# Kernel optimization log

Measured on AMD Instinct MI355X. Metric: run time of the kernel, lower is better.

Reference implementation:

```python
import jax, jax.numpy as jnp
import numpy as np

# Block sizes (DGL message-flow-graph / sampled blocks)
NS0, ND0, NE0 = 300000, 50000, 800000   # block0: 2-hop frontier -> 1-hop frontier
NS1, ND1, NE1 = 50000, 8192, 131072     # block1: 1-hop frontier -> seed nodes


def _graph_conv(x, src, dst, ew, W, b, n_src, n_dst, weight_first):
    """DGL GraphConv with norm='both' and edge_weight.

    x: [n_src, d_in] source-node features; (src, dst): edge endpoints;
    ew: [E] edge weights. Degrees are UNWEIGHTED (copy of DGL semantics),
    clamped to >= 1. Weight applied before aggregation iff d_in > d_out.
    """
    ones_e = jnp.ones_like(ew)
    out_deg = jnp.clip(jax.ops.segment_sum(ones_e, src, num_segments=n_src), 1.0, None)
    h = x * (out_deg ** -0.5)[:, None]
    if weight_first:
        h = h @ W
    # gather-weight-scatter: m_v = sum_{e: e->v} ew_e * h_{src_e}
    msg = jax.ops.segment_sum(ew[:, None] * h[src], dst, num_segments=n_dst)
    in_deg = jnp.clip(jax.ops.segment_sum(ones_e, dst, num_segments=n_dst), 1.0, None)
    msg = msg * (in_deg ** -0.5)[:, None]
    if not weight_first:
        msg = msg @ W
    return msg + b


def setup_inputs() -> dict:
    key = jax.random.key(0)
    ks = jax.random.split(key, 12)
    in_f, hid_f, out_f = 256, 128, 128
    return {
        "x": jax.random.normal(ks[0], (NS0, in_f), dtype=jnp.float32),
        "src0": jax.random.randint(ks[1], (NE0,), 0, NS0, dtype=jnp.int64 if jax.config.jax_enable_x64 else jnp.int32).astype(jnp.int32),
        "dst0": jax.random.randint(ks[2], (NE0,), 0, ND0).astype(jnp.int32),
        "ew0": jax.random.normal(ks[3], (NE0,), dtype=jnp.float32),
        "src1": jax.random.randint(ks[4], (NE1,), 0, NS1).astype(jnp.int32),
        "dst1": jax.random.randint(ks[5], (NE1,), 0, ND1).astype(jnp.int32),
        "ew1": jax.random.normal(ks[6], (NE1,), dtype=jnp.float32),
        "W1": jax.random.normal(ks[7], (in_f, hid_f), dtype=jnp.float32) * 0.05,
        "b1": jax.random.normal(ks[8], (hid_f,), dtype=jnp.float32) * 0.05,
        "W2": jax.random.normal(ks[9], (hid_f, out_f), dtype=jnp.float32) * 0.05,
        "b2": jax.random.normal(ks[10], (out_f,), dtype=jnp.float32) * 0.05,
    }


def reference(x, src0, dst0, ew0, src1, dst1, ew1, W1, b1, W2, b2):
    # layer 1: in(256) > hidden(128) -> weight applied before aggregation
    h = jax.nn.relu(_graph_conv(x, src0, dst0, ew0, W1, b1, NS0, ND0, weight_first=True))
    # layer 2: hidden(128) <= out(128) -> aggregate then weight
    out = jax.nn.relu(_graph_conv(h, src1, dst1, ew1, W2, b2, NS1, ND1, weight_first=False))
    return out  # [ND1, out_f]
```

## Files before the change

### kernel.cpp

```cpp
#include <hip/hip_runtime.h>

#define NS0 300000
#define ND0 50000
#define NE0 800000
#define NS1 50000
#define ND1 8192
#define NE1 131072
#define IN_F 256
#define HID_F 128
#define SLOTS 64
#define NTILE (NS0 / 16)
#define GEMM_GRID 2048
#define BUILD_GRID 512

typedef __attribute__((ext_vector_type(8))) _Float16 half8_t;
typedef __attribute__((ext_vector_type(4))) _Float16 half4_t;
typedef __attribute__((ext_vector_type(4))) float f32x4;

#define OFF_OUTDEG0I 0
#define OFF_OUTDEG1I 300000
#define OFF_CNT0     350000
#define OFF_CNT1     400000
#define ZERO_WORDS   408192
#define OFF_EDGE0    408192
#define OFF_EDGE1    6808192
#define OFF_H1       7856768
#define OFF_W1T      14256768
#define OFF_G        14273152

__global__ __launch_bounds__(256) void k_init(
    int4* __restrict__ p, const float* __restrict__ W1,
    _Float16* __restrict__ w1t) {
  if (blockIdx.x < 128) {
    int i = blockIdx.x * 256 + threadIdx.x;
    for (; i < ZERO_WORDS / 4; i += 128 * 256) p[i] = make_int4(0, 0, 0, 0);
  } else {
    int i = (blockIdx.x - 128) * 256 + threadIdx.x;
    for (; i < IN_F * HID_F; i += 32 * 256) {
      int k = i >> 7, n = i & 127;
      w1t[n * 256 + k] = (_Float16)W1[i];
    }
  }
}

#define LDB(p, o) (*reinterpret_cast<const half8_t*>((p) + (o)))
__global__ __launch_bounds__(256) void k_gemm_build(
    const float* __restrict__ x, const _Float16* __restrict__ w1t,
    _Float16* __restrict__ g,
    const int* __restrict__ src0, const int* __restrict__ dst0,
    const float* __restrict__ ew0, int* __restrict__ outdeg0,
    int* __restrict__ cnt0, int2* __restrict__ edge0,
    const int* __restrict__ src1, const int* __restrict__ dst1,
    const float* __restrict__ ew1, int* __restrict__ outdeg1,
    int* __restrict__ cnt1, int2* __restrict__ edge1) {
  __shared__ __align__(16) _Float16 ldsA[2][16 * 256];
  __shared__ _Float16 ldsT[4][16 * 40];

  if (blockIdx.x >= GEMM_GRID) {
    int tid = (blockIdx.x - GEMM_GRID) * 256 + threadIdx.x;
    int stride = BUILD_GRID * 256;
    for (int i = tid; i < NE0; i += stride) {
      int s = src0[i];
      int d = dst0[i];
      float w = ew0[i];
      atomicAdd(&outdeg0[s], 1);
      int slot = atomicAdd(&cnt0[d], 1);
      if (slot < SLOTS) edge0[d * SLOTS + slot] = make_int2(s, __float_as_int(w));
    }
    for (int i = tid; i < NE1; i += stride) {
      int s = src1[i];
      int d = dst1[i];
      float w = ew1[i];
      atomicAdd(&outdeg1[s], 1);
      int slot = atomicAdd(&cnt1[d], 1);
      if (slot < SLOTS) edge1[d * SLOTS + slot] = make_int2(s, __float_as_int(w));
    }
    return;
  }

  const int tid = threadIdx.x;
  const int wv = tid >> 6;
  const int lane = tid & 63;
  const int m = lane & 15;
  const int grp = lane >> 4;
  _Float16* tp = ldsT[wv];

  const _Float16* wb0 = w1t + (size_t)(32 * wv + m) * 256 + grp * 8;
  const _Float16* wb1 = wb0 + 16 * 256;
  const half8_t b00 = LDB(wb0, 0),   b01 = LDB(wb0, 32),  b02 = LDB(wb0, 64),
                b03 = LDB(wb0, 96),  b04 = LDB(wb0, 128), b05 = LDB(wb0, 160),
                b06 = LDB(wb0, 192), b07 = LDB(wb0, 224);
  const half8_t b10 = LDB(wb1, 0),   b11 = LDB(wb1, 32),  b12 = LDB(wb1, 64),
                b13 = LDB(wb1, 96),  b14 = LDB(wb1, 128), b15 = LDB(wb1, 160),
                b16 = LDB(wb1, 192), b17 = LDB(wb1, 224);

  const int skb = lane >> 3;
  const int sgrp = (lane >> 1) & 3;
  const int sjh = lane & 1;
  const int row_r = lane >> 2;
  const int q_r   = lane & 3;

  const int bid = blockIdx.x;
  float4 pv[4];

  {
    const float* tb = x + (size_t)bid * 4096;
#pragma unroll
    for (int r = 0; r < 4; ++r) {
      const int mr = wv + 4 * r;
      const float4 v = *reinterpret_cast<const float4*>(tb + tid * 4 + r * 1024);
      half4_t h;
      h[0] = (_Float16)v.x; h[1] = (_Float16)v.y;
      h[2] = (_Float16)v.z; h[3] = (_Float16)v.w;
      const int idx = skb * 64 + sgrp * 16 + mr;
      const int S = idx ^ skb ^ sgrp;
      *reinterpret_cast<half4_t*>(
          reinterpret_cast<char*>(&ldsA[0][0]) + S * 16 + sjh * 8) = h;
    }
  }
  __syncthreads();

  int cur = 0;
  for (int tile = bid; tile < NTILE; tile += GEMM_GRID) {
    const int nxt = tile + GEMM_GRID;
    if (nxt < NTILE) {
      const float* tb = x + (size_t)nxt * 4096;
#pragma unroll
      for (int r = 0; r < 4; ++r)
        pv[r] = *reinterpret_cast<const float4*>(tb + tid * 4 + r * 1024);
    }
    {
      const char* A = reinterpret_cast<const char*>(&ldsA[cur][0]);
      f32x4 acc0 = {0.f, 0.f, 0.f, 0.f};
      f32x4 acc1 = {0.f, 0.f, 0.f, 0.f};
#define STEP(KB, B0, B1)                                                       \
  {                                                                            \
    const int Sr = ((KB * 64 + lane) ^ KB ^ grp);                              \
    const half8_t af = *reinterpret_cast<const half8_t*>(A + Sr * 16);         \
    acc0 = __builtin_amdgcn_mfma_f32_16x16x32_f16(af, B0, acc0, 0, 0, 0);      \
    acc1 = __builtin_amdgcn_mfma_f32_16x16x32_f16(af, B1, acc1, 0, 0, 0);      \
  }
      STEP(0, b00, b10)
      STEP(1, b01, b11)
      STEP(2, b02, b12)
      STEP(3, b03, b13)
      STEP(4, b04, b14)
      STEP(5, b05, b15)
      STEP(6, b06, b16)
      STEP(7, b07, b17)
#undef STEP
#pragma unroll
      for (int r = 0; r < 4; ++r) {
        tp[(4 * grp + r) * 40 + m]      = (_Float16)acc0[r];
        tp[(4 * grp + r) * 40 + 16 + m] = (_Float16)acc1[r];
      }
      const half8_t ov =
          *reinterpret_cast<const half8_t*>(tp + row_r * 40 + q_r * 8);
      *reinterpret_cast<half8_t*>(
          g + (size_t)(tile * 16 + row_r) * 128 + 32 * wv + q_r * 8) = ov;
    }
    if (nxt < NTILE) {
      char* B = reinterpret_cast<char*>(&ldsA[cur ^ 1][0]);
#pragma unroll
      for (int r = 0; r < 4; ++r) {
        const int mr = wv + 4 * r;
        half4_t h;
        h[0] = (_Float16)pv[r].x; h[1] = (_Float16)pv[r].y;
        h[2] = (_Float16)pv[r].z; h[3] = (_Float16)pv[r].w;
        const int idx = skb * 64 + sgrp * 16 + mr;
        const int S = idx ^ skb ^ sgrp;
        *reinterpret_cast<half4_t*>(B + S * 16 + sjh * 8) = h;
      }
    }
    __syncthreads();
    cur ^= 1;
  }
}

__global__ __launch_bounds__(256) void k_gather1(
    const _Float16* __restrict__ g, const int* __restrict__ cnt,
    const int2* __restrict__ edge, const int* __restrict__ outdeg0,
    const int* __restrict__ outdeg1, const float* __restrict__ b1,
    float* __restrict__ h1) {
  const int w = (blockIdx.x * 256 + threadIdx.x) >> 6;
  const int lane = threadIdx.x & 63;
  const int gp = lane >> 4;
  const int sl = lane & 15;
  if (w >= ND0) return;
  const int deg = min(cnt[w], SLOTS);
  const int2* ep = edge + (size_t)w * SLOTS;
  float acc[8] = {0.f, 0.f, 0.f, 0.f, 0.f, 0.f, 0.f, 0.f};
  for (int e = 0; e < deg; e += 4) {
    const int idx = e + gp;
    int2 p = make_int2(0, 0);
    float c = 0.f;
    if (idx < deg) {
      p = ep[idx];
      c = __int_as_float(p.y) * rsqrtf(fmaxf((float)outdeg0[p.x], 1.0f));
    }
    const half8_t v =
        *reinterpret_cast<const half8_t*>(g + (size_t)p.x * 128 + sl * 8);
#pragma unroll
    for (int j = 0; j < 8; ++j) acc[j] = fmaf(c, (float)v[j], acc[j]);
  }
#pragma unroll
  for (int j = 0; j < 8; ++j) {
    acc[j] += __shfl_xor(acc[j], 16, 64);
    acc[j] += __shfl_xor(acc[j], 32, 64);
  }
  if (gp == 0) {
    const float sc = rsqrtf(fmaxf((float)deg, 1.0f));
    const float s1 = rsqrtf(fmaxf((float)outdeg1[w], 1.0f));
    const float4 bv0 = *reinterpret_cast<const float4*>(b1 + sl * 8);
    const float4 bv1 = *reinterpret_cast<const float4*>(b1 + sl * 8 + 4);
    float4 o0, o1;
    o0.x = fmaxf(fmaf(acc[0], sc, bv0.x), 0.0f) * s1;
    o0.y = fmaxf(fmaf(acc[1], sc, bv0.y), 0.0f) * s1;
    o0.z = fmaxf(fmaf(acc[2], sc, bv0.z), 0.0f) * s1;
    o0.w = fmaxf(fmaf(acc[3], sc, bv0.w), 0.0f) * s1;
    o1.x = fmaxf(fmaf(acc[4], sc, bv1.x), 0.0f) * s1;
    o1.y = fmaxf(fmaf(acc[5], sc, bv1.y), 0.0f) * s1;
    o1.z = fmaxf(fmaf(acc[6], sc, bv1.z), 0.0f) * s1;
    o1.w = fmaxf(fmaf(acc[7], sc, bv1.w), 0.0f) * s1;
    float* hr = h1 + (size_t)w * 128 + sl * 8;
    *reinterpret_cast<float4*>(hr) = o0;
    *reinterpret_cast<float4*>(hr + 4) = o1;
  }
}

#define FMA2(acc, c, v)        \
  acc.x = fmaf(c, v.x, acc.x); \
  acc.y = fmaf(c, v.y, acc.y);

__global__ __launch_bounds__(256) void k_layer2(
    const float* __restrict__ h1, const int* __restrict__ cnt,
    const int2* __restrict__ edge, const float* __restrict__ W2,
    const float* __restrict__ b2, float* __restrict__ out) {
  __shared__ float arow[8][HID_F];
  const int t = blockIdx.x;
  const int wv = threadIdx.x >> 6;
  const int lane = threadIdx.x & 63;

#pragma unroll
  for (int rr = 0; rr < 2; ++rr) {
    const int row = t * 8 + wv * 2 + rr;
    const int deg = min(cnt[row], SLOTS);
    const int2* ep = edge + (size_t)row * SLOTS;
    float2 acc = make_float2(0.f, 0.f);
    int e = 0;
    for (; e + 4 <= deg; e += 4) {
      int4 q0 = *reinterpret_cast<const int4*>(ep + e);
      int4 q1 = *reinterpret_cast<const int4*>(ep + e + 2);
      float2 v0 = *reinterpret_cast<const float2*>(h1 + (size_t)q0.x * HID_F + lane * 2);
      float2 v1 = *reinterpret_cast<const float2*>(h1 + (size_t)q0.z * HID_F + lane * 2);
      float2 v2 = *reinterpret_cast<const float2*>(h1 + (size_t)q1.x * HID_F + lane * 2);
      float2 v3 = *reinterpret_cast<const float2*>(h1 + (size_t)q1.z * HID_F + lane * 2);
      FMA2(acc, __int_as_float(q0.y), v0);
      FMA2(acc, __int_as_float(q0.w), v1);
      FMA2(acc, __int_as_float(q1.y), v2);
      FMA2(acc, __int_as_float(q1.w), v3);
    }
    for (; e < deg; ++e) {
      int2 p = ep[e];
      float2 v = *reinterpret_cast<const float2*>(h1 + (size_t)p.x * HID_F + lane * 2);
      FMA2(acc, __int_as_float(p.y), v);
    }
    const float sc = rsqrtf(fmaxf((float)deg, 1.0f));
    *reinterpret_cast<float2*>(&arow[wv * 2 + rr][lane * 2]) =
        make_float2(acc.x * sc, acc.y * sc);
  }
  __syncthreads();

  const int j = threadIdx.x & 127;
  const int rg = threadIdx.x >> 7;
  float a0 = 0.f, a1 = 0.f, a2 = 0.f, a3 = 0.f;
  const float* wj = W2 + j;
#pragma unroll 8
  for (int k = 0; k < HID_F; ++k) {
    const float wvv = wj[(size_t)k * 128];
    a0 = fmaf(arow[rg * 4 + 0][k], wvv, a0);
    a1 = fmaf(arow[rg * 4 + 1][k], wvv, a1);
    a2 = fmaf(arow[rg * 4 + 2][k], wvv, a2);
    a3 = fmaf(arow[rg * 4 + 3][k], wvv, a3);
  }
  const float bj = b2[j];
  const int row0 = t * 8 + rg * 4;
  out[(size_t)(row0 + 0) * 128 + j] = fmaxf(a0 + bj, 0.0f);
  out[(size_t)(row0 + 1) * 128 + j] = fmaxf(a1 + bj, 0.0f);
  out[(size_t)(row0 + 2) * 128 + j] = fmaxf(a2 + bj, 0.0f);
  out[(size_t)(row0 + 3) * 128 + j] = fmaxf(a3 + bj, 0.0f);
}

extern "C" void kernel_launch(void* const* d_in, const int* in_sizes, int n_in,
                              void* d_out, int out_size, void* d_ws, size_t ws_size,
                              hipStream_t stream) {
  const float* x    = (const float*)d_in[0];
  const int*   src0 = (const int*)d_in[1];
  const int*   dst0 = (const int*)d_in[2];
  const float* ew0  = (const float*)d_in[3];
  const int*   src1 = (const int*)d_in[4];
  const int*   dst1 = (const int*)d_in[5];
  const float* ew1  = (const float*)d_in[6];
  const float* W1   = (const float*)d_in[7];
  const float* b1   = (const float*)d_in[8];
  const float* W2   = (const float*)d_in[9];
  const float* b2   = (const float*)d_in[10];
  float* out = (float*)d_out;

  int*   wsi = (int*)d_ws;
  float* wsf = (float*)d_ws;
  int* outdeg0 = wsi + OFF_OUTDEG0I;
  int* outdeg1 = wsi + OFF_OUTDEG1I;
  int* cnt0    = wsi + OFF_CNT0;
  int* cnt1    = wsi + OFF_CNT1;
  int2* edge0  = (int2*)(wsi + OFF_EDGE0);
  int2* edge1  = (int2*)(wsi + OFF_EDGE1);
  float* h1    = wsf + OFF_H1;
  _Float16* w1t = (_Float16*)(wsi + OFF_W1T);
  _Float16* g   = (_Float16*)(wsi + OFF_G);

  k_init<<<160, 256, 0, stream>>>((int4*)d_ws, W1, w1t);
  k_gemm_build<<<GEMM_GRID + BUILD_GRID, 256, 0, stream>>>(
      x, w1t, g, src0, dst0, ew0, outdeg0, cnt0, edge0,
      src1, dst1, ew1, outdeg1, cnt1, edge1);
  k_gather1<<<(ND0 * 64) / 256, 256, 0, stream>>>(g, cnt0, edge0, outdeg0,
                                                  outdeg1, b1, h1);
  k_layer2<<<ND1 / 8, 256, 0, stream>>>(h1, cnt1, edge1, W2, b2, out);
}
```

Before: 235.7 us.

## Deepen GEMM prefetch to two tiles ahead and place build blocks first

The GEMM loop now keeps two register buffers of upcoming x tiles, so global loads run two iterations ahead of the MFMA compute instead of one. The loop is unrolled by two with static LDS buffer indices. The edge-build blocks are moved to the low block indices so they are dispatched first and overlap with the GEMM blocks. This costs more registers per thread, which can lower occupancy. The launch grid presumably still covers both roles, though that part is not shown.

```diff
diff --git a/kernel.cpp b/kernel.cpp
--- a/kernel.cpp
+++ b/kernel.cpp
@@ -56,8 +56,8 @@
   __shared__ __align__(16) _Float16 ldsA[2][16 * 256];
   __shared__ _Float16 ldsT[4][16 * 40];
 
-  if (blockIdx.x >= GEMM_GRID) {
-    int tid = (blockIdx.x - GEMM_GRID) * 256 + threadIdx.x;
+  if (blockIdx.x < BUILD_GRID) {
+    int tid = blockIdx.x * 256 + threadIdx.x;
     int stride = BUILD_GRID * 256;
     for (int i = tid; i < NE0; i += stride) {
       int s = src0[i];
@@ -100,8 +100,56 @@
   const int row_r = lane >> 2;
   const int q_r   = lane & 3;
 
-  const int bid = blockIdx.x;
-  float4 pv[4];
+  const int bid = blockIdx.x - BUILD_GRID;
+  float4 pv1[4], pv2[4];
+
+#define LOAD_PV(PV, T)                                                         \
+  {                                                                            \
+    const float* tb = x + (size_t)(T) * 4096;                                  \
+    _Pragma("unroll") for (int r = 0; r < 4; ++r)                              \
+        PV[r] = *reinterpret_cast<const float4*>(tb + tid * 4 + r * 1024);     \
+  }
+
+#define WRITE_LDS(BUFI, PV)                                                    \
+  {                                                                            \
+    char* Bp = reinterpret_cast<char*>(&ldsA[BUFI][0]);                        \
+    _Pragma("unroll") for (int r = 0; r < 4; ++r) {                            \
+      const int mr = wv + 4 * r;                                               \
+      half4_t h;                                                               \
+      h[0] = (_Float16)PV[r].x; h[1] = (_Float16)PV[r].y;                      \
+      h[2] = (_Float16)PV[r].z; h[3] = (_Float16)PV[r].w;                      \
+      const int idx = skb * 64 + sgrp * 16 + mr;                               \
+      const int S = idx ^ skb ^ sgrp;                                          \
+      *reinterpret_cast<half4_t*>(Bp + S * 16 + sjh * 8) = h;                  \
+    }                                                                          \
+  }
+
+#define STEP(A, KB, B0, B1)                                                    \
+  {                                                                            \
+    const int Sr = ((KB * 64 + lane) ^ KB ^ grp);                              \
+    const half8_t af = *reinterpret_cast<const half8_t*>(A + Sr * 16);         \
+    acc0 = __builtin_amdgcn_mfma_f32_16x16x32_f16(af, B0, acc0, 0, 0, 0);      \
+    acc1 = __builtin_amdgcn_mfma_f32_16x16x32_f16(af, B1, acc1, 0, 0, 0);      \
+  }
+
+#define COMPUTE_TILE(BUFI, T)                                                  \
+  {                                                                            \
+    const char* A = reinterpret_cast<const char*>(&ldsA[BUFI][0]);             \
+    f32x4 acc0 = {0.f, 0.f, 0.f, 0.f};                                         \
+    f32x4 acc1 = {0.f, 0.f, 0.f, 0.f};                                         \
+    STEP(A, 0, b00, b10) STEP(A, 1, b01, b11)                                  \
+    STEP(A, 2, b02, b12) STEP(A, 3, b03, b13)                                  \
+    STEP(A, 4, b04, b14) STEP(A, 5, b05, b15)                                  \
+    STEP(A, 6, b06, b16) STEP(A, 7, b07, b17)                                  \
+    _Pragma("unroll") for (int r = 0; r < 4; ++r) {                            \
+      tp[(4 * grp + r) * 40 + m]      = (_Float16)acc0[r];                     \
+      tp[(4 * grp + r) * 40 + 16 + m] = (_Float16)acc1[r];                     \
+    }                                                                          \
+    const half8_t ov =                                                         \
+        *reinterpret_cast<const half8_t*>(tp + row_r * 40 + q_r * 8);          \
+    *reinterpret_cast<half8_t*>(                                               \
+        g + (size_t)((T) * 16 + row_r) * 128 + 32 * wv + q_r * 8) = ov;        \
+  }
 
   {
     const float* tb = x + (size_t)bid * 4096;
@@ -118,63 +166,28 @@
           reinterpret_cast<char*>(&ldsA[0][0]) + S * 16 + sjh * 8) = h;
     }
   }
+  if (bid + GEMM_GRID < NTILE) LOAD_PV(pv1, bid + GEMM_GRID);
   __syncthreads();
 
-  int cur = 0;
-  for (int tile = bid; tile < NTILE; tile += GEMM_GRID) {
-    const int nxt = tile + GEMM_GRID;
-    if (nxt < NTILE) {
-      const float* tb = x + (size_t)nxt * 4096;
-#pragma unroll
-      for (int r = 0; r < 4; ++r)
-        pv[r] = *reinterpret_cast<const float4*>(tb + tid * 4 + r * 1024);
-    }
-    {
-      const char* A = reinterpret_cast<const char*>(&ldsA[cur][0]);
-      f32x4 acc0 = {0.f, 0.f, 0.f, 0.f};
-      f32x4 acc1 = {0.f, 0.f, 0.f, 0.f};
-#define STEP(KB, B0, B1)                                                       \
-  {                                                                            \
-    const int Sr = ((KB * 64 + lane) ^ KB ^ grp);                              \
-    const half8_t af = *reinterpret_cast<const half8_t*>(A + Sr * 16);         \
-    acc0 = __builtin_amdgcn_mfma_f32_16x16x32_f16(af, B0, acc0, 0, 0, 0);      \
-    acc1 = __builtin_amdgcn_mfma_f32_16x16x32_f16(af, B1, acc1, 0, 0, 0);      \
-  }
-      STEP(0, b00, b10)
-      STEP(1, b01, b11)
-      STEP(2, b02, b12)
-      STEP(3, b03, b13)
-      STEP(4, b04, b14)
-      STEP(5, b05, b15)
-      STEP(6, b06, b16)
-      STEP(7, b07, b17)
+  for (int t = bid; t < NTILE; t += 2 * GEMM_GRID) {
+    const int tA2 = t + 2 * GEMM_GRID;
+    if (tA2 < NTILE) LOAD_PV(pv2, tA2);
+    COMPUTE_TILE(0, t);
+    if (t + GEMM_GRID < NTILE) WRITE_LDS(1, pv1);
+    __syncthreads();
+    const int tB = t + GEMM_GRID;
+    if (tB < NTILE) {
+      const int tB3 = t + 3 * GEMM_GRID;
+      if (tB3 < NTILE) LOAD_PV(pv1, tB3);
+      COMPUTE_TILE(1, tB);
+      if (tA2 < NTILE) WRITE_LDS(0, pv2);
+      __syncthreads();
+    }
+  }
+#undef LOAD_PV
+#undef WRITE_LDS
 #undef STEP
-#pragma unroll
-      for (int r = 0; r < 4; ++r) {
-        tp[(4 * grp + r) * 40 + m]      = (_Float16)acc0[r];
-        tp[(4 * grp + r) * 40 + 16 + m] = (_Float16)acc1[r];
-      }
-      const half8_t ov =
-          *reinterpret_cast<const half8_t*>(tp + row_r * 40 + q_r * 8);
-      *reinterpret_cast<half8_t*>(
-          g + (size_t)(tile * 16 + row_r) * 128 + 32 * wv + q_r * 8) = ov;
-    }
-    if (nxt < NTILE) {
-      char* B = reinterpret_cast<char*>(&ldsA[cur ^ 1][0]);
-#pragma unroll
-      for (int r = 0; r < 4; ++r) {
-        const int mr = wv + 4 * r;
-        half4_t h;
-        h[0] = (_Float16)pv[r].x; h[1] = (_Float16)pv[r].y;
-        h[2] = (_Float16)pv[r].z; h[3] = (_Float16)pv[r].w;
-        const int idx = skb * 64 + sgrp * 16 + mr;
-        const int S = idx ^ skb ^ sgrp;
-        *reinterpret_cast<half4_t*>(B + S * 16 + sjh * 8) = h;
-      }
-    }
-    __syncthreads();
-    cur ^= 1;
-  }
+#undef COMPUTE_TILE
 }
 
 __global__ __launch_bounds__(256) void k_gather1(
```

Result: faster. 229.8 us (median of 2 runs) (-2.5%).

## Make GEMM wave-independent with per-wave 16-row tiles and fused edge build

Applied to the files above, without the earlier changes.

The layer-1 X·W1 GEMM is restructured so that each wavefront owns a whole 16-row tile and computes all 128 output columns. B fragments come from a pre-swizzled fp16 W1 layout in global memory/L2 rather than being held in registers. This removes the block-wide double buffer and __syncthreads. The edge-bucket build, which used to run in separate blocks, is now done by every block before its GEMM work. The trade-offs are more global loads of B per tile, no cross-tile prefetch, and atomic-heavy edge work serialized ahead of the GEMM inside each block.

```diff
diff --git a/kernel.cpp b/kernel.cpp
--- a/kernel.cpp
+++ b/kernel.cpp
@@ -10,8 +10,8 @@
 #define HID_F 128
 #define SLOTS 64
 #define NTILE (NS0 / 16)
-#define GEMM_GRID 2048
-#define BUILD_GRID 512
+#define GRID 2048
+#define TPLD 136
 
 typedef __attribute__((ext_vector_type(8))) _Float16 half8_t;
 typedef __attribute__((ext_vector_type(4))) _Float16 half4_t;
@@ -25,27 +25,31 @@
 #define OFF_EDGE0    408192
 #define OFF_EDGE1    6808192
 #define OFF_H1       7856768
-#define OFF_W1T      14256768
+#define OFF_W1X      14256768
 #define OFF_G        14273152
 
 __global__ __launch_bounds__(256) void k_init(
     int4* __restrict__ p, const float* __restrict__ W1,
-    _Float16* __restrict__ w1t) {
+    _Float16* __restrict__ w1x) {
   if (blockIdx.x < 128) {
     int i = blockIdx.x * 256 + threadIdx.x;
     for (; i < ZERO_WORDS / 4; i += 128 * 256) p[i] = make_int4(0, 0, 0, 0);
   } else {
-    int i = (blockIdx.x - 128) * 256 + threadIdx.x;
-    for (; i < IN_F * HID_F; i += 32 * 256) {
-      int k = i >> 7, n = i & 127;
-      w1t[n * 256 + k] = (_Float16)W1[i];
-    }
-  }
-}
-
-#define LDB(p, o) (*reinterpret_cast<const half8_t*>((p) + (o)))
-__global__ __launch_bounds__(256) void k_gemm_build(
-    const float* __restrict__ x, const _Float16* __restrict__ w1t,
+    int f = (blockIdx.x - 128) * 256 + threadIdx.x;
+    for (; f < IN_F * HID_F; f += 32 * 256) {
+      const int ct = f >> 12;
+      const int kb = (f >> 9) & 7;
+      const int grpm = (f >> 3) & 63;
+      const int j = f & 7;
+      const int n = ct * 16 + (grpm & 15);
+      const int k = kb * 32 + (grpm >> 4) * 8 + j;
+      w1x[f] = (_Float16)W1[k * 128 + n];
+    }
+  }
+}
+
+__global__ __launch_bounds__(256) void k_gemm_wave(
+    const float* __restrict__ x, const _Float16* __restrict__ w1x,
     _Float16* __restrict__ g,
     const int* __restrict__ src0, const int* __restrict__ dst0,
     const float* __restrict__ ew0, int* __restrict__ outdeg0,
@@ -53,13 +57,23 @@
     const int* __restrict__ src1, const int* __restrict__ dst1,
     const float* __restrict__ ew1, int* __restrict__ outdeg1,
     int* __restrict__ cnt1, int2* __restrict__ edge1) {
-  __shared__ __align__(16) _Float16 ldsA[2][16 * 256];
-  __shared__ _Float16 ldsT[4][16 * 40];
-
-  if (blockIdx.x >= GEMM_GRID) {
-    int tid = (blockIdx.x - GEMM_GRID) * 256 + threadIdx.x;
-    int stride = BUILD_GRID * 256;
-    for (int i = tid; i < NE0; i += stride) {
+  __shared__ __align__(16) _Float16 patchA[4][16 * 256];
+  __shared__ __align__(16) _Float16 tpT[4][16 * TPLD];
+  const int tid = threadIdx.x;
+  const int wv = tid >> 6;
+  const int lane = tid & 63;
+  const int grp = lane >> 4;
+  const int m = lane & 15;
+  const int skb = lane >> 3;
+  const int sgrp = (lane >> 1) & 3;
+  const int sjh = lane & 1;
+  const int sidx_base = skb * 64 + sgrp * 16;
+  const int sxor = skb ^ sgrp;
+
+  {
+    const int gl = blockIdx.x * 256 + tid;
+    const int total = GRID * 256;
+    for (int i = gl; i < NE0; i += total) {
       int s = src0[i];
       int d = dst0[i];
       float w = ew0[i];
@@ -67,7 +81,7 @@
       int slot = atomicAdd(&cnt0[d], 1);
       if (slot < SLOTS) edge0[d * SLOTS + slot] = make_int2(s, __float_as_int(w));
     }
-    for (int i = tid; i < NE1; i += stride) {
+    for (int i = gl; i < NE1; i += total) {
       int s = src1[i];
       int d = dst1[i];
       float w = ew1[i];
@@ -75,105 +89,50 @@
       int slot = atomicAdd(&cnt1[d], 1);
       if (slot < SLOTS) edge1[d * SLOTS + slot] = make_int2(s, __float_as_int(w));
     }
-    return;
-  }
-
-  const int tid = threadIdx.x;
-  const int wv = tid >> 6;
-  const int lane = tid & 63;
-  const int m = lane & 15;
-  const int grp = lane >> 4;
-  _Float16* tp = ldsT[wv];
-
-  const _Float16* wb0 = w1t + (size_t)(32 * wv + m) * 256 + grp * 8;
-  const _Float16* wb1 = wb0 + 16 * 256;
-  const half8_t b00 = LDB(wb0, 0),   b01 = LDB(wb0, 32),  b02 = LDB(wb0, 64),
-                b03 = LDB(wb0, 96),  b04 = LDB(wb0, 128), b05 = LDB(wb0, 160),
-                b06 = LDB(wb0, 192), b07 = LDB(wb0, 224);
-  const half8_t b10 = LDB(wb1, 0),   b11 = LDB(wb1, 32),  b12 = LDB(wb1, 64),
-                b13 = LDB(wb1, 96),  b14 = LDB(wb1, 128), b15 = LDB(wb1, 160),
-                b16 = LDB(wb1, 192), b17 = LDB(wb1, 224);
-
-  const int skb = lane >> 3;
-  const int sgrp = (lane >> 1) & 3;
-  const int sjh = lane & 1;
-  const int row_r = lane >> 2;
-  const int q_r   = lane & 3;
-
-  const int bid = blockIdx.x;
-  float4 pv[4];
-
-  {
-    const float* tb = x + (size_t)bid * 4096;
-#pragma unroll
-    for (int r = 0; r < 4; ++r) {
-      const int mr = wv + 4 * r;
-      const float4 v = *reinterpret_cast<const float4*>(tb + tid * 4 + r * 1024);
+  }
+
+  char* pa = reinterpret_cast<char*>(&patchA[wv][0]);
+  _Float16* tp = &tpT[wv][0];
+  const int gw = blockIdx.x * 4 + wv;
+
+  for (int T = gw; T < NTILE; T += GRID * 4) {
+    const float* xb = x + (size_t)T * 4096;
+#pragma unroll
+    for (int t = 0; t < 16; ++t) {
+      const float4 v = *reinterpret_cast<const float4*>(xb + t * 256 + lane * 4);
       half4_t h;
       h[0] = (_Float16)v.x; h[1] = (_Float16)v.y;
       h[2] = (_Float16)v.z; h[3] = (_Float16)v.w;
-      const int idx = skb * 64 + sgrp * 16 + mr;
-      const int S = idx ^ skb ^ sgrp;
-      *reinterpret_cast<half4_t*>(
-          reinterpret_cast<char*>(&ldsA[0][0]) + S * 16 + sjh * 8) = h;
-    }
-  }
-  __syncthreads();
-
-  int cur = 0;
-  for (int tile = bid; tile < NTILE; tile += GEMM_GRID) {
-    const int nxt = tile + GEMM_GRID;
-    if (nxt < NTILE) {
-      const float* tb = x + (size_t)nxt * 4096;
+      const int S = (sidx_base + t) ^ sxor;
+      *reinterpret_cast<half4_t*>(pa + S * 16 + sjh * 8) = h;
+    }
+    f32x4 acc[8];
+#pragma unroll
+    for (int ct = 0; ct < 8; ++ct) acc[ct] = (f32x4){0.f, 0.f, 0.f, 0.f};
+#pragma unroll
+    for (int kb = 0; kb < 8; ++kb) {
+      const int Sr = (kb * 64 + lane) ^ kb ^ grp;
+      const half8_t af = *reinterpret_cast<const half8_t*>(pa + Sr * 16);
+#pragma unroll
+      for (int ct = 0; ct < 8; ++ct) {
+        const half8_t bf = *reinterpret_cast<const half8_t*>(
+            w1x + (size_t)(ct * 8 + kb) * 512 + lane * 8);
+        acc[ct] = __builtin_amdgcn_mfma_f32_16x16x32_f16(af, bf, acc[ct], 0, 0, 0);
+      }
+    }
+#pragma unroll
+    for (int ct = 0; ct < 8; ++ct)
 #pragma unroll
       for (int r = 0; r < 4; ++r)
-        pv[r] = *reinterpret_cast<const float4*>(tb + tid * 4 + r * 1024);
-    }
-    {
-      const char* A = reinterpret_cast<const char*>(&ldsA[cur][0]);
-      f32x4 acc0 = {0.f, 0.f, 0.f, 0.f};
-      f32x4 acc1 = {0.f, 0.f, 0.f, 0.f};
-#define STEP(KB, B0, B1)                                                       \
-  {                                                                            \
-    const int Sr = ((KB * 64 + lane) ^ KB ^ grp);                              \
-    const half8_t af = *reinterpret_cast<const half8_t*>(A + Sr * 16);         \
-    acc0 = __builtin_amdgcn_mfma_f32_16x16x32_f16(af, B0, acc0, 0, 0, 0);      \
-    acc1 = __builtin_amdgcn_mfma_f32_16x16x32_f16(af, B1, acc1, 0, 0, 0);      \
-  }
-      STEP(0, b00, b10)
-      STEP(1, b01, b11)
-      STEP(2, b02, b12)
-      STEP(3, b03, b13)
-      STEP(4, b04, b14)
-      STEP(5, b05, b15)
-      STEP(6, b06, b16)
-      STEP(7, b07, b17)
-#undef STEP
-#pragma unroll
-      for (int r = 0; r < 4; ++r) {
-        tp[(4 * grp + r) * 40 + m]      = (_Float16)acc0[r];
-        tp[(4 * grp + r) * 40 + 16 + m] = (_Float16)acc1[r];
-      }
+        tp[(4 * grp + r) * TPLD + ct * 16 + m] = (_Float16)acc[ct][r];
+#pragma unroll
+    for (int q = 0; q < 4; ++q) {
+      const int row = q * 4 + grp;
       const half8_t ov =
-          *reinterpret_cast<const half8_t*>(tp + row_r * 40 + q_r * 8);
+          *reinterpret_cast<const half8_t*>(tp + row * TPLD + m * 8);
       *reinterpret_cast<half8_t*>(
-          g + (size_t)(tile * 16 + row_r) * 128 + 32 * wv + q_r * 8) = ov;
-    }
-    if (nxt < NTILE) {
-      char* B = reinterpret_cast<char*>(&ldsA[cur ^ 1][0]);
-#pragma unroll
-      for (int r = 0; r < 4; ++r) {
-        const int mr = wv + 4 * r;
-        half4_t h;
-        h[0] = (_Float16)pv[r].x; h[1] = (_Float16)pv[r].y;
-        h[2] = (_Float16)pv[r].z; h[3] = (_Float16)pv[r].w;
-        const int idx = skb * 64 + sgrp * 16 + mr;
-        const int S = idx ^ skb ^ sgrp;
-        *reinterpret_cast<half4_t*>(B + S * 16 + sjh * 8) = h;
-      }
-    }
-    __syncthreads();
-    cur ^= 1;
+          g + ((size_t)T * 16 + row) * 128 + m * 8) = ov;
+    }
   }
 }
 
@@ -316,12 +275,12 @@
   int2* edge0  = (int2*)(wsi + OFF_EDGE0);
   int2* edge1  = (int2*)(wsi + OFF_EDGE1);
   float* h1    = wsf + OFF_H1;
-  _Float16* w1t = (_Float16*)(wsi + OFF_W1T);
+  _Float16* w1x = (_Float16*)(wsi + OFF_W1X);
   _Float16* g   = (_Float16*)(wsi + OFF_G);
 
-  k_init<<<160, 256, 0, stream>>>((int4*)d_ws, W1, w1t);
-  k_gemm_build<<<GEMM_GRID + BUILD_GRID, 256, 0, stream>>>(
-      x, w1t, g, src0, dst0, ew0, outdeg0, cnt0, edge0,
+  k_init<<<160, 256, 0, stream>>>((int4*)d_ws, W1, w1x);
+  k_gemm_wave<<<GRID, 256, 0, stream>>>(
+      x, w1x, g, src0, dst0, ew0, outdeg0, cnt0, edge0,
       src1, dst1, ew1, outdeg1, cnt1, edge1);
   k_gather1<<<(ND0 * 64) / 256, 256, 0, stream>>>(g, cnt0, edge0, outdeg0,
                                                   outdeg1, b1, h1);
```

After: 341.8 us (median of 2 runs). 45.0% more time.

## Launch one GEMM block per 16-row tile and put build blocks first

Applied to the files above, without the earlier changes.

Replaces the persistent, double-buffered GEMM loop (2048 blocks striding over tiles with register prefetch) with one block per 16-row tile (18750 blocks), each loading, converting, multiplying and storing exactly once. Edge-build blocks now come first in the grid so they are scheduled early instead of after all GEMM blocks. This removes the software pipelining and the loop overhead and relies on hardware block scheduling and occupancy to hide latency. The cost is that every block reloads the 16 B-fragment registers of W1 and pays launch overhead.

```diff
diff --git a/kernel.cpp b/kernel.cpp
--- a/kernel.cpp
+++ b/kernel.cpp
@@ -9,8 +9,7 @@
 #define IN_F 256
 #define HID_F 128
 #define SLOTS 64
-#define NTILE (NS0 / 16)
-#define GEMM_GRID 2048
+#define NT16 (NS0 / 16)
 #define BUILD_GRID 512
 
 typedef __attribute__((ext_vector_type(8))) _Float16 half8_t;
@@ -53,11 +52,11 @@
     const int* __restrict__ src1, const int* __restrict__ dst1,
     const float* __restrict__ ew1, int* __restrict__ outdeg1,
     int* __restrict__ cnt1, int2* __restrict__ edge1) {
-  __shared__ __align__(16) _Float16 ldsA[2][16 * 256];
+  __shared__ __align__(16) _Float16 ldsA[16 * 256];
   __shared__ _Float16 ldsT[4][16 * 40];
 
-  if (blockIdx.x >= GEMM_GRID) {
-    int tid = (blockIdx.x - GEMM_GRID) * 256 + threadIdx.x;
+  if (blockIdx.x < BUILD_GRID) {
+    int tid = blockIdx.x * 256 + threadIdx.x;
     int stride = BUILD_GRID * 256;
     for (int i = tid; i < NE0; i += stride) {
       int s = src0[i];
@@ -85,6 +84,30 @@
   const int grp = lane >> 4;
   _Float16* tp = ldsT[wv];
 
+  const int skb = lane >> 3;
+  const int sgrp = (lane >> 1) & 3;
+  const int sjh = lane & 1;
+  const int row_r = lane >> 2;
+  const int q_r   = lane & 3;
+
+  const int T = blockIdx.x - BUILD_GRID;
+
+  {
+    const float* tb = x + (size_t)T * 4096;
+    char* Bp = reinterpret_cast<char*>(&ldsA[0]);
+#pragma unroll
+    for (int r = 0; r < 4; ++r) {
+      const float4 v = *reinterpret_cast<const float4*>(tb + tid * 4 + r * 1024);
+      const int mr = wv + 4 * r;
+      half4_t hv;
+      hv[0] = (_Float16)v.x; hv[1] = (_Float16)v.y;
+      hv[2] = (_Float16)v.z; hv[3] = (_Float16)v.w;
+      const int idx = skb * 64 + sgrp * 16 + mr;
+      const int S = idx ^ skb ^ sgrp;
+      *reinterpret_cast<half4_t*>(Bp + S * 16 + sjh * 8) = hv;
+    }
+  }
+
   const _Float16* wb0 = w1t + (size_t)(32 * wv + m) * 256 + grp * 8;
   const _Float16* wb1 = wb0 + 16 * 256;
   const half8_t b00 = LDB(wb0, 0),   b01 = LDB(wb0, 32),  b02 = LDB(wb0, 64),
@@ -94,45 +117,11 @@
                 b13 = LDB(wb1, 96),  b14 = LDB(wb1, 128), b15 = LDB(wb1, 160),
                 b16 = LDB(wb1, 192), b17 = LDB(wb1, 224);
 
-  const int skb = lane >> 3;
-  const int sgrp = (lane >> 1) & 3;
-  const int sjh = lane & 1;
-  const int row_r = lane >> 2;
-  const int q_r   = lane & 3;
-
-  const int bid = blockIdx.x;
-  float4 pv[4];
-
-  {
-    const float* tb = x + (size_t)bid * 4096;
-#pragma unroll
-    for (int r = 0; r < 4; ++r) {
-      const int mr = wv + 4 * r;
-      const float4 v = *reinterpret_cast<const float4*>(tb + tid * 4 + r * 1024);
-      half4_t h;
-      h[0] = (_Float16)v.x; h[1] = (_Float16)v.y;
-      h[2] = (_Float16)v.z; h[3] = (_Float16)v.w;
-      const int idx = skb * 64 + sgrp * 16 + mr;
-      const int S = idx ^ skb ^ sgrp;
-      *reinterpret_cast<half4_t*>(
-          reinterpret_cast<char*>(&ldsA[0][0]) + S * 16 + sjh * 8) = h;
-    }
-  }
   __syncthreads();
 
-  int cur = 0;
-  for (int tile = bid; tile < NTILE; tile += GEMM_GRID) {
-    const int nxt = tile + GEMM_GRID;
-    if (nxt < NTILE) {
-      const float* tb = x + (size_t)nxt * 4096;
-#pragma unroll
-      for (int r = 0; r < 4; ++r)
-        pv[r] = *reinterpret_cast<const float4*>(tb + tid * 4 + r * 1024);
-    }
-    {
-      const char* A = reinterpret_cast<const char*>(&ldsA[cur][0]);
-      f32x4 acc0 = {0.f, 0.f, 0.f, 0.f};
-      f32x4 acc1 = {0.f, 0.f, 0.f, 0.f};
+  const char* A = reinterpret_cast<const char*>(&ldsA[0]);
+  f32x4 acc0 = {0.f, 0.f, 0.f, 0.f};
+  f32x4 acc1 = {0.f, 0.f, 0.f, 0.f};
 #define STEP(KB, B0, B1)                                                       \
   {                                                                            \
     const int Sr = ((KB * 64 + lane) ^ KB ^ grp);                              \
@@ -140,41 +129,24 @@
     acc0 = __builtin_amdgcn_mfma_f32_16x16x32_f16(af, B0, acc0, 0, 0, 0);      \
     acc1 = __builtin_amdgcn_mfma_f32_16x16x32_f16(af, B1, acc1, 0, 0, 0);      \
   }
-      STEP(0, b00, b10)
-      STEP(1, b01, b11)
-      STEP(2, b02, b12)
-      STEP(3, b03, b13)
-      STEP(4, b04, b14)
-      STEP(5, b05, b15)
-      STEP(6, b06, b16)
-      STEP(7, b07, b17)
+  STEP(0, b00, b10)
+  STEP(1, b01, b11)
+  STEP(2, b02, b12)
+  STEP(3, b03, b13)
+  STEP(4, b04, b14)
+  STEP(5, b05, b15)
+  STEP(6, b06, b16)
+  STEP(7, b07, b17)
 #undef STEP
-#pragma unroll
-      for (int r = 0; r < 4; ++r) {
-        tp[(4 * grp + r) * 40 + m]      = (_Float16)acc0[r];
-        tp[(4 * grp + r) * 40 + 16 + m] = (_Float16)acc1[r];
-      }
-      const half8_t ov =
-          *reinterpret_cast<const half8_t*>(tp + row_r * 40 + q_r * 8);
-      *reinterpret_cast<half8_t*>(
-          g + (size_t)(tile * 16 + row_r) * 128 + 32 * wv + q_r * 8) = ov;
-    }
-    if (nxt < NTILE) {
-      char* B = reinterpret_cast<char*>(&ldsA[cur ^ 1][0]);
-#pragma unroll
-      for (int r = 0; r < 4; ++r) {
-        const int mr = wv + 4 * r;
-        half4_t h;
-        h[0] = (_Float16)pv[r].x; h[1] = (_Float16)pv[r].y;
-        h[2] = (_Float16)pv[r].z; h[3] = (_Float16)pv[r].w;
-        const int idx = skb * 64 + sgrp * 16 + mr;
-        const int S = idx ^ skb ^ sgrp;
-        *reinterpret_cast<half4_t*>(B + S * 16 + sjh * 8) = h;
-      }
-    }
-    __syncthreads();
-    cur ^= 1;
-  }
+
+#pragma unroll
+  for (int r = 0; r < 4; ++r) {
+    tp[(4 * grp + r) * 40 + m]      = (_Float16)acc0[r];
+    tp[(4 * grp + r) * 40 + 16 + m] = (_Float16)acc1[r];
+  }
+  const half8_t ov = *reinterpret_cast<const half8_t*>(tp + row_r * 40 + q_r * 8);
+  *reinterpret_cast<half8_t*>(
+      g + ((size_t)T * 16 + row_r) * 128 + 32 * wv + q_r * 8) = ov;
 }
 
 __global__ __launch_bounds__(256) void k_gather1(
@@ -320,7 +292,7 @@
   _Float16* g   = (_Float16*)(wsi + OFF_G);
 
   k_init<<<160, 256, 0, stream>>>((int4*)d_ws, W1, w1t);
-  k_gemm_build<<<GEMM_GRID + BUILD_GRID, 256, 0, stream>>>(
+  k_gemm_build<<<BUILD_GRID + NT16, 256, 0, stream>>>(
       x, w1t, g, src0, dst0, ew0, outdeg0, cnt0, edge0,
       src1, dst1, ew1, outdeg1, cnt1, edge1);
   k_gather1<<<(ND0 * 64) / 256, 256, 0, stream>>>(g, cnt0, edge0, outdeg0,
```

Measured after the change: 304.4 us. 1.29x slower.
